# Kernel optimization log

Hardware: AMD Instinct MI355X
Metric: run time of the kernel (lower is better)

Reference implementation:

```python
import jax, jax.numpy as jnp
import numpy as np

B, T, C = 4, 4096, 512


def setup_inputs() -> dict:
    key = jax.random.key(0)
    ks = jax.random.split(key, 7)
    s = 1.0 / np.sqrt(C)  # ~ torch Linear init scale
    X = jax.random.normal(ks[0], (B, T, C), jnp.float32)
    S_n = jnp.zeros((B, C, C), jnp.float32)
    W_Q = jax.random.normal(ks[1], (C, C), jnp.float32) * s
    b_Q = jax.random.normal(ks[2], (C,), jnp.float32) * s
    W_K = jax.random.normal(ks[3], (C, C), jnp.float32) * s
    b_K = jax.random.normal(ks[4], (C,), jnp.float32) * s
    W_V = jax.random.normal(ks[5], (C, C), jnp.float32) * s
    b_V = jax.random.normal(ks[6], (C,), jnp.float32) * s
    return {"X": X, "S_n": S_n, "W_Q": W_Q, "b_Q": b_Q,
            "W_K": W_K, "b_K": b_K, "W_V": W_V, "b_V": b_V}


def reference(X, S_n, W_Q, b_Q, W_K, b_K, W_V, b_V):
    # forward_chunkwise with chunk_len = 1 (exact simplification):
    #   per step t (gamma g_t from linspace(0.96, 0.99, T)):
    #     inner_t = (q_t . k_t) * v_t            # D = gamma^0 = 1
    #     cross_t = (q_t @ S) * g_t              # e[:,0,:] = g^1
    #     O_t     = tanh(inner_t + cross_t)
    #     S      <- k_t^T v_t + g_t * S          # D[-1] = 1, g**chunk_len = g
    Bx, Tx, Cx = X.shape
    Q = X @ W_Q + b_Q  # [B,T,C]
    K = X @ W_K + b_K
    V = X @ W_V + b_V
    gammas = jnp.linspace(0.96, 0.99, Tx).astype(X.dtype)

    def step(S, inp):
        q, k, v, g = inp  # q,k,v: [B,C]; g: scalar
        inner = jnp.sum(q * k, axis=-1, keepdims=True) * v      # [B,C]
        cross = jnp.einsum('bc,bcd->bd', q, S) * g              # [B,C]
        O = jnp.tanh(inner + cross)
        S_new = jnp.einsum('bc,bd->bcd', k, v) + S * g          # [B,C,C]
        return S_new, O

    # original resets S_n to zeros regardless of the passed-in value
    S0 = jnp.zeros_like(S_n)
    S_final, O = jax.lax.scan(
        step, S0,
        (Q.transpose(1, 0, 2), K.transpose(1, 0, 2), V.transpose(1, 0, 2), gammas))
    out = O.transpose(1, 0, 2)  # [B,T,C]
    return out, S_final
```

## Files before the change

kernel.cpp:

```cpp
#include <hip/hip_runtime.h>
#include <math.h>

#define Bsz  4
#define Tlen 4096
#define Cdim 512
#define CUT  (-12.0f)
#define NBE  8388608

typedef unsigned int u32;
typedef _Float16 f16;
typedef __attribute__((ext_vector_type(8))) _Float16 f16x8;
typedef __attribute__((ext_vector_type(4))) float floatx4;
#define MFMA_F16(a,b,c) __builtin_amdgcn_mfma_f32_16x16x32_f16((a),(b),(c),0,0,0)

union pun8 { uint4 u; f16x8 f; };

__device__ __forceinline__ u32 pack2(f16 a, f16 b) {
    return (u32)__builtin_bit_cast(unsigned short, a) |
           ((u32)__builtin_bit_cast(unsigned short, b) << 16);
}
__device__ __forceinline__ u32 splitpack(float v) {
    f16 h = (f16)v;
    f16 l = (f16)(v - (float)h);
    return pack2(h, l);
}
__device__ __forceinline__ void unpack8(const u32* p, f16x8& h, f16x8& l) {
    uint4 q0 = *(const uint4*)p;
    uint4 q1 = *(const uint4*)(p + 4);
    pun8 ph, pl;
    ph.u.x = __builtin_amdgcn_perm(q0.y, q0.x, 0x05040100u);
    pl.u.x = __builtin_amdgcn_perm(q0.y, q0.x, 0x07060302u);
    ph.u.y = __builtin_amdgcn_perm(q0.w, q0.z, 0x05040100u);
    pl.u.y = __builtin_amdgcn_perm(q0.w, q0.z, 0x07060302u);
    ph.u.z = __builtin_amdgcn_perm(q1.y, q1.x, 0x05040100u);
    pl.u.z = __builtin_amdgcn_perm(q1.y, q1.x, 0x07060302u);
    ph.u.w = __builtin_amdgcn_perm(q1.w, q1.z, 0x05040100u);
    pl.u.w = __builtin_amdgcn_perm(q1.w, q1.z, 0x07060302u);
    h = ph.f; l = pl.f;
}
__device__ __forceinline__ float tanh_fast(float x) {
    return 1.0f - 2.0f / (__expf(2.0f * x) + 1.0f);
}

__global__ __launch_bounds__(256) void prep_kernel(
    const float* __restrict__ X,
    const float* __restrict__ WQ, const float* __restrict__ WK,
    const float* __restrict__ WV,
    f16* __restrict__ Xf, f16* __restrict__ WT,
    float* __restrict__ Lg, float* __restrict__ Wfin, int* __restrict__ sLo) {
    __shared__ char pshm[18432];
    int bid = blockIdx.x, tid = threadIdx.x;
    if (bid < 2048) {
        size_t i = ((size_t)bid * 256 + tid) * 16;
        float v[16];
#pragma unroll
        for (int j = 0; j < 4; ++j) {
            float4 a = *(const float4*)(X + i + j * 4);
            v[j*4+0]=a.x; v[j*4+1]=a.y; v[j*4+2]=a.z; v[j*4+3]=a.w;
        }
        uint4 o0, o1;
        o0.x = pack2((f16)v[0], (f16)v[1]);   o0.y = pack2((f16)v[2], (f16)v[3]);
        o0.z = pack2((f16)v[4], (f16)v[5]);   o0.w = pack2((f16)v[6], (f16)v[7]);
        o1.x = pack2((f16)v[8], (f16)v[9]);   o1.y = pack2((f16)v[10], (f16)v[11]);
        o1.z = pack2((f16)v[12], (f16)v[13]); o1.w = pack2((f16)v[14], (f16)v[15]);
        *(uint4*)(Xf + i) = o0;
        *(uint4*)(Xf + i + 8) = o1;
    } else if (bid < 2240) {
        f16* tile = (f16*)pshm;
        int wb = bid - 2048;
        int mat = wb >> 6, rem = wb & 63;
        int k0 = (rem >> 3) * 64, n0 = (rem & 7) * 64;
        const float* W = (mat == 0) ? WQ : (mat == 1) ? WK : WV;
        int row = tid >> 2, q = tid & 3;
        const float* src = W + (size_t)(k0 + row) * Cdim + n0 + q * 16;
        float vv[16];
#pragma unroll
        for (int j = 0; j < 4; ++j) {
            float4 v = *(const float4*)(src + j * 4);
            vv[j*4+0]=v.x; vv[j*4+1]=v.y; vv[j*4+2]=v.z; vv[j*4+3]=v.w;
        }
#pragma unroll
        for (int j = 0; j < 16; ++j) tile[(q * 16 + j) * 72 + row] = (f16)vv[j];
        __syncthreads();
        f16x8 r0 = *(const f16x8*)(tile + row * 72 + q * 16);
        f16x8 r1 = *(const f16x8*)(tile + row * 72 + q * 16 + 8);
        f16* dst = WT + ((size_t)mat * Cdim + n0 + row) * Cdim + k0 + q * 16;
        *(f16x8*)dst = r0;
        *(f16x8*)(dst + 8) = r1;
    } else {
        float* Lsh = (float*)pshm;
        float* sums = (float*)(pshm + 16400);
        float lg[16];
        float local = 0.f;
        int base = tid * 16;
#pragma unroll
        for (int i = 0; i < 16; ++i) {
            int t = base + i;
            float g = 0.96f + 0.03f * ((float)t * (1.0f / 4095.0f));
            lg[i] = logf(g);
            local += lg[i];
        }
        sums[tid] = local;
        __syncthreads();
        for (int off = 1; off < 256; off <<= 1) {
            float v = sums[tid];
            if (tid >= off) v += sums[tid - off];
            __syncthreads();
            sums[tid] = v;
            __syncthreads();
        }
        float pre = (tid == 0) ? 0.f : sums[tid - 1];
#pragma unroll
        for (int i = 0; i < 16; ++i) {
            Lsh[base + i] = pre;
            pre += lg[i];
        }
        if (tid == 255) Lsh[4096] = pre;
        __syncthreads();
        for (int t = tid; t < 4097; t += 256) Lg[t] = Lsh[t];
        float LT = Lsh[4096];
        for (int s = tid; s < 4096; s += 256) Wfin[s] = __expf(LT - Lsh[s + 1]);
        if (tid < 64) {
            float ref = Lsh[tid * 64 + 1];
            int st_hi = tid >> 1;
            int lo = st_hi;
            for (int st = 0; st < st_hi; ++st)
                if (ref - Lsh[st * 128 + 128] > CUT) { lo = st; break; }
            sLo[tid] = lo;
        }
    }
}

__global__ __launch_bounds__(256, 2) void qkv_mfma(
    const f16* __restrict__ Xf, const f16* __restrict__ WT,
    const float* __restrict__ bQ, const float* __restrict__ bK,
    const float* __restrict__ bV,
    f16* __restrict__ Qf, f16* __restrict__ Kf,
    f16* __restrict__ KT, f16* __restrict__ VT) {
    __shared__ char smem[34816];
    u32* sX = (u32*)smem;
    u32* sW = (u32*)(smem + 16384);
    f16* sB = (f16*)smem;

    int tid = threadIdx.x, lane = tid & 63, wid = tid >> 6;
    int l16 = lane & 15, quad = lane >> 4;
    int wm = wid & 1, wn = wid >> 1;
    int xb = blockIdx.x;
    int mat = xb >> 2, n0 = (xb & 3) * 128;
    int m0 = blockIdx.y * 128;

    floatx4 acc[4][4];
#pragma unroll
    for (int i = 0; i < 4; ++i)
#pragma unroll
        for (int j = 0; j < 4; ++j) acc[i][j] = (floatx4)0.f;

    int srow = tid >> 1, shalf = tid & 1;
    int arow_a = wm * 64 + l16, arow_b = wn * 64 + l16;
    int swz_f = (l16 & 7) << 2;

    for (int kc = 0; kc < Cdim; kc += 64) {
        __syncthreads();
        {
            const f16* gx = Xf + (size_t)(m0 + srow) * Cdim + kc + shalf * 32;
            const f16* gw = WT + ((size_t)(mat * Cdim) + n0 + srow) * Cdim + kc + shalf * 32;
            int wswz = (srow & 7) << 2;
#pragma unroll
            for (int k = 0; k < 4; ++k) {
                uint4 xv = *(const uint4*)(gx + k * 8);
                uint4 wv = *(const uint4*)(gw + k * 8);
                int w = shalf * 16 + k * 4;
                *(uint4*)&sX[srow * 32 + (w ^ wswz)] = xv;
                *(uint4*)&sW[srow * 32 + (w ^ wswz)] = wv;
            }
        }
        __syncthreads();
#pragma unroll
        for (int ks = 0; ks < 2; ++ks) {
            int w0 = ks * 16 + quad * 4;
            f16x8 af[4], bf[4];
#pragma unroll
            for (int mt = 0; mt < 4; ++mt)
                af[mt] = ((pun8*)&sX[(arow_a + mt * 16) * 32 + (w0 ^ swz_f)])->f;
#pragma unroll
            for (int nt = 0; nt < 4; ++nt)
                bf[nt] = ((pun8*)&sW[(arow_b + nt * 16) * 32 + (w0 ^ swz_f)])->f;
#pragma unroll
            for (int mt = 0; mt < 4; ++mt)
#pragma unroll
                for (int nt = 0; nt < 4; ++nt)
                    acc[mt][nt] = MFMA_F16(af[mt], bf[nt], acc[mt][nt]);
        }
    }

    const float* bias = (mat == 0) ? bQ : (mat == 1) ? bK : bV;
    float bv[4];
#pragma unroll
    for (int nt = 0; nt < 4; ++nt) bv[nt] = bias[n0 + wn * 64 + nt * 16 + l16];
    float cv[4][4][4];
#pragma unroll
    for (int mt = 0; mt < 4; ++mt)
#pragma unroll
        for (int nt = 0; nt < 4; ++nt)
#pragma unroll
            for (int r = 0; r < 4; ++r) cv[mt][nt][r] = acc[mt][nt][r] + bv[nt];

    int b = m0 >> 12, tloc = m0 & 4095;

    if (mat == 2) {
#pragma unroll
        for (int mt = 0; mt < 4; ++mt)
#pragma unroll
            for (int nt = 0; nt < 4; ++nt) {
                int d = n0 + wn * 64 + nt * 16 + l16;
                int t = tloc + wm * 64 + mt * 16 + quad * 4;
                uint2 w;
                w.x = pack2((f16)cv[mt][nt][0], (f16)cv[mt][nt][1]);
                w.y = pack2((f16)cv[mt][nt][2], (f16)cv[mt][nt][3]);
                *(uint2*)(VT + ((size_t)(b * Cdim + d)) * Tlen + t) = w;
            }
    } else {
        if (mat == 1) {
#pragma unroll
            for (int mt = 0; mt < 4; ++mt)
#pragma unroll
                for (int nt = 0; nt < 4; ++nt) {
                    int d = n0 + wn * 64 + nt * 16 + l16;
                    int t = tloc + wm * 64 + mt * 16 + quad * 4;
                    uint2 w;
                    w.x = pack2((f16)cv[mt][nt][0], (f16)cv[mt][nt][1]);
                    w.y = pack2((f16)cv[mt][nt][2], (f16)cv[mt][nt][3]);
                    *(uint2*)(KT + ((size_t)(b * Cdim + d)) * Tlen + t) = w;
                }
        }
        __syncthreads();
#pragma unroll
        for (int mt = 0; mt < 4; ++mt)
#pragma unroll
            for (int nt = 0; nt < 4; ++nt)
#pragma unroll
                for (int r = 0; r < 4; ++r)
                    sB[(wm * 64 + mt * 16 + quad * 4 + r) * 136 +
                       wn * 64 + nt * 16 + l16] = (f16)cv[mt][nt][r];
        __syncthreads();
        {
            f16* Out = (mat == 0) ? Qf : Kf;
            int r2 = tid >> 1, h2 = tid & 1;
            f16* dst = Out + (size_t)(m0 + r2) * Cdim + n0 + h2 * 64;
#pragma unroll
            for (int j = 0; j < 8; ++j)
                *(uint4*)(dst + j * 8) = *(const uint4*)(sB + r2 * 136 + h2 * 64 + j * 8);
        }
    }
}

__global__ __launch_bounds__(512, 2) void attn_mfma(
    const f16* __restrict__ Qf, const f16* __restrict__ Kf,
    const f16* __restrict__ VT, const float* __restrict__ Lg,
    const int* __restrict__ sLo, float* __restrict__ out) {
    __shared__ char smem[99328];
    u32* sQ  = (u32*)smem;
    u32* sPc = (u32*)(smem + 65536);

    int tid = threadIdx.x, lane = tid & 63, wid = tid >> 6;
    int l16 = lane & 15, quad = lane >> 4;
    int mw = wid & 1;
    int nw = wid >> 1;

    int x = blockIdx.x & 7, j = blockIdx.x >> 3;
    int b = x >> 1;
    int tt = (j << 1) | (x & 1);
    int t0 = tt * 64;
    size_t bT = (size_t)b * Tlen;
    int lo = sLo[tt], hi = tt >> 1;

    {
        int r = tid >> 3, c8 = tid & 7;
        const f16* src = Qf + (bT + t0 + r) * Cdim + c8 * 64;
        int wswz = (r & 7) << 2;
#pragma unroll
        for (int k = 0; k < 8; ++k) {
            uint4 v = *(const uint4*)(src + k * 8);
            int w = c8 * 32 + k * 4;
            *(uint4*)&sQ[r * 256 + (w ^ wswz)] = v;
        }
    }

    float aT[2][4];
#pragma unroll
    for (int mt = 0; mt < 2; ++mt)
#pragma unroll
        for (int r = 0; r < 4; ++r)
            aT[mt][r] = Lg[t0 + mw * 32 + mt * 16 + quad * 4 + r + 1];

    floatx4 oacc[2][8];
#pragma unroll
    for (int i = 0; i < 2; ++i)
#pragma unroll
        for (int jj = 0; jj < 8; ++jj) oacc[i][jj] = (floatx4)0.f;

    int swz_f = (l16 & 7) << 2;
    int rowA0 = (mw * 32 + l16) * 256;
    int rowA1 = (mw * 32 + 16 + l16) * 256;

    __syncthreads();

    for (int st = lo; st <= hi; ++st) {
        int s0 = st * 128;
        float lsp[2];
#pragma unroll
        for (int sq = 0; sq < 2; ++sq)
            lsp[sq] = Lg[s0 + nw * 32 + sq * 16 + l16 + 1];

        floatx4 pacc[2][2];
#pragma unroll
        for (int i = 0; i < 2; ++i)
#pragma unroll
            for (int jj = 0; jj < 2; ++jj) pacc[i][jj] = (floatx4)0.f;

        const f16* kb = Kf + (bT + s0 + nw * 32 + l16) * Cdim;
#pragma unroll 4
        for (int kc = 0; kc < 16; ++kc) {
            int ko = kc * 32 + quad * 8;
            int w0 = kc * 16 + quad * 4;
            f16x8 a0 = ((pun8*)&sQ[rowA0 + (w0 ^ swz_f)])->f;
            f16x8 a1 = ((pun8*)&sQ[rowA1 + (w0 ^ swz_f)])->f;
            f16x8 b0 = *(const f16x8*)(kb + ko);
            f16x8 b1 = *(const f16x8*)(kb + 16 * Cdim + ko);
            pacc[0][0] = MFMA_F16(a0, b0, pacc[0][0]);
            pacc[0][1] = MFMA_F16(a0, b1, pacc[0][1]);
            pacc[1][0] = MFMA_F16(a1, b0, pacc[1][0]);
            pacc[1][1] = MFMA_F16(a1, b1, pacc[1][1]);
        }

        __syncthreads();
#pragma unroll
        for (int mt = 0; mt < 2; ++mt)
#pragma unroll
            for (int sq = 0; sq < 2; ++sq)
#pragma unroll
                for (int r = 0; r < 4; ++r) {
                    int tl = mw * 32 + mt * 16 + quad * 4 + r;
                    int sl = nw * 32 + sq * 16 + l16;
                    int t = t0 + tl, s = s0 + sl;
                    float p = pacc[mt][sq][r];
                    p = (s <= t) ? p * __expf(aT[mt][r] - lsp[sq]) : 0.f;
                    sPc[tl * 132 + (sl ^ ((tl & 7) << 4))] = splitpack(p);
                }
        __syncthreads();

        const f16* vb = VT + ((size_t)(b * Cdim + nw * 128 + l16)) * Tlen + s0;
#pragma unroll
        for (int kf = 0; kf < 4; ++kf) {
            int sb = kf * 32 + quad * 8;
            f16x8 ph[2], pl[2];
#pragma unroll
            for (int mt = 0; mt < 2; ++mt) {
                int tl = mw * 32 + mt * 16 + l16;
                unpack8(&sPc[tl * 132 + (sb ^ ((tl & 7) << 4))], ph[mt], pl[mt]);
            }
#pragma unroll
            for (int nt = 0; nt < 8; ++nt) {
                f16x8 vf = *(const f16x8*)(vb + (size_t)nt * 16 * Tlen + sb);
#pragma unroll
                for (int mt = 0; mt < 2; ++mt) {
                    oacc[mt][nt] = MFMA_F16(ph[mt], vf, oacc[mt][nt]);
                    oacc[mt][nt] = MFMA_F16(pl[mt], vf, oacc[mt][nt]);
                }
            }
        }
    }

#pragma unroll
    for (int mt = 0; mt < 2; ++mt)
#pragma unroll
        for (int nt = 0; nt < 8; ++nt)
#pragma unroll
            for (int r = 0; r < 4; ++r) {
                int t = t0 + mw * 32 + mt * 16 + quad * 4 + r;
                int d = nw * 128 + nt * 16 + l16;
                out[(bT + t) * (size_t)Cdim + d] = tanh_fast(oacc[mt][nt][r]);
            }
}

__global__ __launch_bounds__(256) void sfinal_mfma(
    const f16* __restrict__ KT, const f16* __restrict__ VT,
    const float* __restrict__ Lg, const float* __restrict__ Wfin,
    float* __restrict__ S) {
    __shared__ f16 sA[64 * 72];
    __shared__ f16 sB2[64 * 72];
    int tid = threadIdx.x, lane = tid & 63, wid = tid >> 6;
    int l16 = lane & 15, quad = lane >> 4;
    int wv_c = wid & 1, wv_d = wid >> 1;
    int c0 = blockIdx.x * 64, d0 = blockIdx.y * 64, b = blockIdx.z;
    float LT = Lg[Tlen];
    floatx4 acc[2][2];
#pragma unroll
    for (int i = 0; i < 2; ++i)
#pragma unroll
        for (int jj = 0; jj < 2; ++jj) acc[i][jj] = (floatx4)0.f;

    int s0start = Tlen - 64;
    for (int s0 = 0; s0 < Tlen; s0 += 64)
        if (LT - Lg[s0 + 64] > CUT) { s0start = s0; break; }

    int row = tid >> 2, q = tid & 3;
    for (int s0 = s0start; s0 < Tlen; s0 += 64) {
        __syncthreads();
        {
            const f16* g = KT + ((size_t)(b * Cdim + c0 + row)) * Tlen + s0 + q * 16;
            f16x8 u0 = *(const f16x8*)g;
            f16x8 u1 = *(const f16x8*)(g + 8);
            float wv[16];
#pragma unroll
            for (int jj = 0; jj < 4; ++jj) {
                float4 w4 = *(const float4*)(Wfin + s0 + q * 16 + jj * 4);
                wv[jj*4+0]=w4.x; wv[jj*4+1]=w4.y; wv[jj*4+2]=w4.z; wv[jj*4+3]=w4.w;
            }
            f16x8 o0, o1;
#pragma unroll
            for (int jj = 0; jj < 8; ++jj) o0[jj] = (f16)((float)u0[jj] * wv[jj]);
#pragma unroll
            for (int jj = 0; jj < 8; ++jj) o1[jj] = (f16)((float)u1[jj] * wv[8 + jj]);
            *(f16x8*)(sA + row * 72 + q * 16) = o0;
            *(f16x8*)(sA + row * 72 + q * 16 + 8) = o1;
            const f16* gv = VT + ((size_t)(b * Cdim + d0 + row)) * Tlen + s0 + q * 16;
            uint4 v0 = *(const uint4*)gv, v1 = *(const uint4*)(gv + 8);
            *(uint4*)(sB2 + row * 72 + q * 16) = v0;
            *(uint4*)(sB2 + row * 72 + q * 16 + 8) = v1;
        }
        __syncthreads();
#pragma unroll
        for (int ks = 0; ks < 2; ++ks) {
            int ko = ks * 32 + quad * 8;
            f16x8 a0 = *(const f16x8*)(sA + (wv_c * 32 + l16) * 72 + ko);
            f16x8 a1 = *(const f16x8*)(sA + (wv_c * 32 + 16 + l16) * 72 + ko);
            f16x8 b0 = *(const f16x8*)(sB2 + (wv_d * 32 + l16) * 72 + ko);
            f16x8 b1 = *(const f16x8*)(sB2 + (wv_d * 32 + 16 + l16) * 72 + ko);
            acc[0][0] = MFMA_F16(a0, b0, acc[0][0]);
            acc[0][1] = MFMA_F16(a0, b1, acc[0][1]);
            acc[1][0] = MFMA_F16(a1, b0, acc[1][0]);
            acc[1][1] = MFMA_F16(a1, b1, acc[1][1]);
        }
    }
#pragma unroll
    for (int ct = 0; ct < 2; ++ct)
#pragma unroll
        for (int dt = 0; dt < 2; ++dt)
#pragma unroll
            for (int r = 0; r < 4; ++r) {
                int c = c0 + wv_c * 32 + ct * 16 + quad * 4 + r;
                int d = d0 + wv_d * 32 + dt * 16 + l16;
                S[((size_t)(b * Cdim + c)) * Cdim + d] = acc[ct][dt][r];
            }
}

extern "C" void kernel_launch(void* const* d_in, const int* in_sizes, int n_in,
                              void* d_out, int out_size, void* d_ws, size_t ws_size,
                              hipStream_t stream) {
    (void)in_sizes; (void)n_in; (void)out_size; (void)ws_size;
    const float* X  = (const float*)d_in[0];
    const float* WQ = (const float*)d_in[2];
    const float* bQ = (const float*)d_in[3];
    const float* WK = (const float*)d_in[4];
    const float* bK = (const float*)d_in[5];
    const float* WV = (const float*)d_in[6];
    const float* bV = (const float*)d_in[7];

    float* out   = (float*)d_out;
    float* S_out = out + (size_t)NBE;

    char* ws = (char*)d_ws;
    f16*   Xf   = (f16*)(ws);
    f16*   Qf   = (f16*)(ws + 2ull * NBE);
    f16*   Kf   = (f16*)(ws + 4ull * NBE);
    f16*   KT   = (f16*)(ws + 6ull * NBE);
    f16*   VT   = (f16*)(ws + 8ull * NBE);
    f16*   WT   = (f16*)(ws + 10ull * NBE);
    char*  tail = ws + 10ull * NBE + (2u << 20);
    float* Lg   = (float*)(tail);
    float* Wfin = (float*)(tail + 16512);
    int*   sLo  = (int*)(tail + 16512 + 16384);

    prep_kernel<<<2241, 256, 0, stream>>>(X, WQ, WK, WV, Xf, WT, Lg, Wfin, sLo);
    qkv_mfma<<<dim3(12, 128), 256, 0, stream>>>(Xf, WT, bQ, bK, bV, Qf, Kf, KT, VT);
    attn_mfma<<<256, 512, 0, stream>>>(Qf, Kf, VT, Lg, sLo, out);
    sfinal_mfma<<<dim3(8, 8, Bsz), 256, 0, stream>>>(KT, VT, Lg, Wfin, S_out);
}
```

Baseline: 301.4 us.

## Halve attention query tile, drop split-fp16 P, reorder blocks longest-first

The attention kernel now processes 32 query rows per block instead of 64, launching twice as many blocks with much less shared memory so more blocks can be resident per CU. The block-to-tile mapping is now ordered longest-first (paired from both ends) to balance the causal workload. The P matrix is stored as a single fp16 value instead of a hi/lo split pair, halving the second-GEMM MFMA count, and P uses a double buffer so one barrier per step is removed. The cost is reduced precision in the P·V product, and each K/V tile is reloaded by twice as many blocks.

```diff
diff --git a/kernel.cpp b/kernel.cpp
--- a/kernel.cpp
+++ b/kernel.cpp
@@ -8,6 +8,7 @@
 #define NBE  8388608
 
 typedef unsigned int u32;
+typedef unsigned short u16;
 typedef _Float16 f16;
 typedef __attribute__((ext_vector_type(8))) _Float16 f16x8;
 typedef __attribute__((ext_vector_type(4))) float floatx4;
@@ -16,27 +17,8 @@
 union pun8 { uint4 u; f16x8 f; };
 
 __device__ __forceinline__ u32 pack2(f16 a, f16 b) {
-    return (u32)__builtin_bit_cast(unsigned short, a) |
-           ((u32)__builtin_bit_cast(unsigned short, b) << 16);
-}
-__device__ __forceinline__ u32 splitpack(float v) {
-    f16 h = (f16)v;
-    f16 l = (f16)(v - (float)h);
-    return pack2(h, l);
-}
-__device__ __forceinline__ void unpack8(const u32* p, f16x8& h, f16x8& l) {
-    uint4 q0 = *(const uint4*)p;
-    uint4 q1 = *(const uint4*)(p + 4);
-    pun8 ph, pl;
-    ph.u.x = __builtin_amdgcn_perm(q0.y, q0.x, 0x05040100u);
-    pl.u.x = __builtin_amdgcn_perm(q0.y, q0.x, 0x07060302u);
-    ph.u.y = __builtin_amdgcn_perm(q0.w, q0.z, 0x05040100u);
-    pl.u.y = __builtin_amdgcn_perm(q0.w, q0.z, 0x07060302u);
-    ph.u.z = __builtin_amdgcn_perm(q1.y, q1.x, 0x05040100u);
-    pl.u.z = __builtin_amdgcn_perm(q1.y, q1.x, 0x07060302u);
-    ph.u.w = __builtin_amdgcn_perm(q1.w, q1.z, 0x05040100u);
-    pl.u.w = __builtin_amdgcn_perm(q1.w, q1.z, 0x07060302u);
-    h = ph.f; l = pl.f;
+    return (u32)__builtin_bit_cast(u16, a) |
+           ((u32)__builtin_bit_cast(u16, b) << 16);
 }
 __device__ __forceinline__ float tanh_fast(float x) {
     return 1.0f - 2.0f / (__expf(2.0f * x) + 1.0f);
@@ -47,7 +29,8 @@
     const float* __restrict__ WQ, const float* __restrict__ WK,
     const float* __restrict__ WV,
     f16* __restrict__ Xf, f16* __restrict__ WT,
-    float* __restrict__ Lg, float* __restrict__ Wfin, int* __restrict__ sLo) {
+    float* __restrict__ Lg, float* __restrict__ Wfin,
+    int* __restrict__ sLo) {
     __shared__ char pshm[18432];
     int bid = blockIdx.x, tid = threadIdx.x;
     if (bid < 2048) {
@@ -120,9 +103,9 @@
         for (int t = tid; t < 4097; t += 256) Lg[t] = Lsh[t];
         float LT = Lsh[4096];
         for (int s = tid; s < 4096; s += 256) Wfin[s] = __expf(LT - Lsh[s + 1]);
-        if (tid < 64) {
-            float ref = Lsh[tid * 64 + 1];
-            int st_hi = tid >> 1;
+        if (tid < 128) {
+            float ref = Lsh[tid * 32 + 1];
+            int st_hi = tid >> 2;
             int lo = st_hi;
             for (int st = 0; st < st_hi; ++st)
                 if (ref - Lsh[st * 128 + 128] > CUT) { lo = st; break; }
@@ -254,133 +237,114 @@
     }
 }
 
-__global__ __launch_bounds__(512, 2) void attn_mfma(
+__global__ __launch_bounds__(512, 4) void attn_mfma(
     const f16* __restrict__ Qf, const f16* __restrict__ Kf,
     const f16* __restrict__ VT, const float* __restrict__ Lg,
     const int* __restrict__ sLo, float* __restrict__ out) {
-    __shared__ char smem[99328];
-    u32* sQ  = (u32*)smem;
-    u32* sPc = (u32*)(smem + 65536);
+    __shared__ u32 sQ[32 * 256];
+    __shared__ u32 sP[2][32 * 64];
 
     int tid = threadIdx.x, lane = tid & 63, wid = tid >> 6;
     int l16 = lane & 15, quad = lane >> 4;
     int mw = wid & 1;
     int nw = wid >> 1;
 
-    int x = blockIdx.x & 7, j = blockIdx.x >> 3;
-    int b = x >> 1;
-    int tt = (j << 1) | (x & 1);
-    int t0 = tt * 64;
+    int i = blockIdx.x;
+    int rnk = (i < 256) ? i : 767 - i;
+    int tt = 127 - (rnk >> 2);
+    int b = rnk & 3;
+    int t0 = tt * 32;
     size_t bT = (size_t)b * Tlen;
-    int lo = sLo[tt], hi = tt >> 1;
+    int lo = sLo[tt], hi = tt >> 2;
 
     {
-        int r = tid >> 3, c8 = tid & 7;
-        const f16* src = Qf + (bT + t0 + r) * Cdim + c8 * 64;
-        int wswz = (r & 7) << 2;
-#pragma unroll
-        for (int k = 0; k < 8; ++k) {
-            uint4 v = *(const uint4*)(src + k * 8);
-            int w = c8 * 32 + k * 4;
-            *(uint4*)&sQ[r * 256 + (w ^ wswz)] = v;
-        }
-    }
-
-    float aT[2][4];
-#pragma unroll
-    for (int mt = 0; mt < 2; ++mt)
-#pragma unroll
-        for (int r = 0; r < 4; ++r)
-            aT[mt][r] = Lg[t0 + mw * 32 + mt * 16 + quad * 4 + r + 1];
-
-    floatx4 oacc[2][8];
-#pragma unroll
-    for (int i = 0; i < 2; ++i)
-#pragma unroll
-        for (int jj = 0; jj < 8; ++jj) oacc[i][jj] = (floatx4)0.f;
-
-    int swz_f = (l16 & 7) << 2;
-    int rowA0 = (mw * 32 + l16) * 256;
-    int rowA1 = (mw * 32 + 16 + l16) * 256;
+        int r = tid >> 4, c = tid & 15;
+        const f16* src = Qf + (bT + t0 + r) * Cdim + c * 32;
+        int r7 = r & 7;
+        u32* dst = sQ + r * 256;
+        uint4 v0 = *(const uint4*)src;
+        uint4 v1 = *(const uint4*)(src + 8);
+        uint4 v2 = *(const uint4*)(src + 16);
+        uint4 v3 = *(const uint4*)(src + 24);
+        *(uint4*)&dst[((c * 4 + 0) ^ r7) << 2] = v0;
+        *(uint4*)&dst[((c * 4 + 1) ^ r7) << 2] = v1;
+        *(uint4*)&dst[((c * 4 + 2) ^ r7) << 2] = v2;
+        *(uint4*)&dst[((c * 4 + 3) ^ r7) << 2] = v3;
+    }
+
+    float aT[4];
+#pragma unroll
+    for (int r = 0; r < 4; ++r)
+        aT[r] = Lg[t0 + mw * 16 + quad * 4 + r + 1];
+
+    floatx4 oacc[8];
+#pragma unroll
+    for (int jj = 0; jj < 8; ++jj) oacc[jj] = (floatx4)0.f;
 
     __syncthreads();
 
-    for (int st = lo; st <= hi; ++st) {
+    int pbuf = 0;
+    for (int st = lo; st <= hi; ++st, pbuf ^= 1) {
         int s0 = st * 128;
         float lsp[2];
 #pragma unroll
         for (int sq = 0; sq < 2; ++sq)
             lsp[sq] = Lg[s0 + nw * 32 + sq * 16 + l16 + 1];
 
-        floatx4 pacc[2][2];
-#pragma unroll
-        for (int i = 0; i < 2; ++i)
-#pragma unroll
-            for (int jj = 0; jj < 2; ++jj) pacc[i][jj] = (floatx4)0.f;
+        floatx4 pacc[2];
+        pacc[0] = (floatx4)0.f; pacc[1] = (floatx4)0.f;
 
         const f16* kb = Kf + (bT + s0 + nw * 32 + l16) * Cdim;
+        const u32* qrow = sQ + (mw * 16 + l16) * 256;
+        int r7 = l16 & 7;
 #pragma unroll 4
         for (int kc = 0; kc < 16; ++kc) {
-            int ko = kc * 32 + quad * 8;
-            int w0 = kc * 16 + quad * 4;
-            f16x8 a0 = ((pun8*)&sQ[rowA0 + (w0 ^ swz_f)])->f;
-            f16x8 a1 = ((pun8*)&sQ[rowA1 + (w0 ^ swz_f)])->f;
-            f16x8 b0 = *(const f16x8*)(kb + ko);
-            f16x8 b1 = *(const f16x8*)(kb + 16 * Cdim + ko);
-            pacc[0][0] = MFMA_F16(a0, b0, pacc[0][0]);
-            pacc[0][1] = MFMA_F16(a0, b1, pacc[0][1]);
-            pacc[1][0] = MFMA_F16(a1, b0, pacc[1][0]);
-            pacc[1][1] = MFMA_F16(a1, b1, pacc[1][1]);
-        }
-
-        __syncthreads();
-#pragma unroll
-        for (int mt = 0; mt < 2; ++mt)
-#pragma unroll
-            for (int sq = 0; sq < 2; ++sq)
-#pragma unroll
-                for (int r = 0; r < 4; ++r) {
-                    int tl = mw * 32 + mt * 16 + quad * 4 + r;
-                    int sl = nw * 32 + sq * 16 + l16;
-                    int t = t0 + tl, s = s0 + sl;
-                    float p = pacc[mt][sq][r];
-                    p = (s <= t) ? p * __expf(aT[mt][r] - lsp[sq]) : 0.f;
-                    sPc[tl * 132 + (sl ^ ((tl & 7) << 4))] = splitpack(p);
-                }
+            f16x8 a = ((const pun8*)&qrow[((kc * 4 + quad) ^ r7) << 2])->f;
+            f16x8 b0 = *(const f16x8*)(kb + kc * 32 + quad * 8);
+            f16x8 b1 = *(const f16x8*)(kb + 16 * Cdim + kc * 32 + quad * 8);
+            pacc[0] = MFMA_F16(a, b0, pacc[0]);
+            pacc[1] = MFMA_F16(a, b1, pacc[1]);
+        }
+
+        f16* sPp = (f16*)sP[pbuf];
+#pragma unroll
+        for (int sq = 0; sq < 2; ++sq)
+#pragma unroll
+            for (int r = 0; r < 4; ++r) {
+                int tl = mw * 16 + quad * 4 + r;
+                int sl = nw * 32 + sq * 16 + l16;
+                int t = t0 + tl, s = s0 + sl;
+                float p = pacc[sq][r];
+                p = (s <= t) ? p * __expf(aT[r] - lsp[sq]) : 0.f;
+                int i16 = tl * 128 + ((((sl >> 3) ^ (tl & 7)) << 3) | (sl & 7));
+                sPp[i16] = (f16)p;
+            }
         __syncthreads();
 
         const f16* vb = VT + ((size_t)(b * Cdim + nw * 128 + l16)) * Tlen + s0;
+        const f16* sPf = (const f16*)sP[pbuf];
+        int rowP = mw * 16 + l16;
+        int rp7 = rowP & 7;
 #pragma unroll
         for (int kf = 0; kf < 4; ++kf) {
             int sb = kf * 32 + quad * 8;
-            f16x8 ph[2], pl[2];
-#pragma unroll
-            for (int mt = 0; mt < 2; ++mt) {
-                int tl = mw * 32 + mt * 16 + l16;
-                unpack8(&sPc[tl * 132 + (sb ^ ((tl & 7) << 4))], ph[mt], pl[mt]);
-            }
+            f16x8 pa = *(const f16x8*)&sPf[rowP * 128 + ((((sb >> 3) ^ rp7) << 3))];
 #pragma unroll
             for (int nt = 0; nt < 8; ++nt) {
                 f16x8 vf = *(const f16x8*)(vb + (size_t)nt * 16 * Tlen + sb);
-#pragma unroll
-                for (int mt = 0; mt < 2; ++mt) {
-                    oacc[mt][nt] = MFMA_F16(ph[mt], vf, oacc[mt][nt]);
-                    oacc[mt][nt] = MFMA_F16(pl[mt], vf, oacc[mt][nt]);
-                }
-            }
-        }
-    }
-
-#pragma unroll
-    for (int mt = 0; mt < 2; ++mt)
-#pragma unroll
-        for (int nt = 0; nt < 8; ++nt)
-#pragma unroll
-            for (int r = 0; r < 4; ++r) {
-                int t = t0 + mw * 32 + mt * 16 + quad * 4 + r;
-                int d = nw * 128 + nt * 16 + l16;
-                out[(bT + t) * (size_t)Cdim + d] = tanh_fast(oacc[mt][nt][r]);
-            }
+                oacc[nt] = MFMA_F16(pa, vf, oacc[nt]);
+            }
+        }
+    }
+
+#pragma unroll
+    for (int nt = 0; nt < 8; ++nt)
+#pragma unroll
+        for (int r = 0; r < 4; ++r) {
+            int t = t0 + mw * 16 + quad * 4 + r;
+            int d = nw * 128 + nt * 16 + l16;
+            out[(bT + t) * (size_t)Cdim + d] = tanh_fast(oacc[nt][r]);
+        }
 }
 
 __global__ __launch_bounds__(256) void sfinal_mfma(
@@ -484,6 +448,6 @@
 
     prep_kernel<<<2241, 256, 0, stream>>>(X, WQ, WK, WV, Xf, WT, Lg, Wfin, sLo);
     qkv_mfma<<<dim3(12, 128), 256, 0, stream>>>(Xf, WT, bQ, bK, bV, Qf, Kf, KT, VT);
-    attn_mfma<<<256, 512, 0, stream>>>(Qf, Kf, VT, Lg, sLo, out);
+    attn_mfma<<<512, 512, 0, stream>>>(Qf, Kf, VT, Lg, sLo, out);
     sfinal_mfma<<<dim3(8, 8, Bsz), 256, 0, stream>>>(KT, VT, Lg, Wfin, S_out);
 }
```

Result: slower. 332.7 us (+10.4%).
